# Kernel tuning notes

Hardware: AMD Instinct MI355X
Metric: run time of the kernel (lower is better)

The kernel has to match this reference:

```python
import jax, jax.numpy as jnp
import numpy as np

N = 131072   # number of profile points
S = 64       # n_samples (PSF samples per point)
D = H = W = 256


def setup_inputs() -> dict:
    key = jax.random.key(0)
    k1, k2, k3, k4, k5, k6 = jax.random.split(key, 6)
    x = jax.random.normal(k1, (1, 1, D, H, W), dtype=jnp.float32)
    # voxel-space coordinates (x, y, z) inside the volume
    sampleGrid = jax.random.uniform(k2, (N, 3), dtype=jnp.float32) * jnp.array(
        [W - 1, H - 1, D - 1], dtype=jnp.float32)
    # small axis-angle rotations + translations: [N, 1, 6]
    rot = jax.random.normal(k3, (N, 1, 3), dtype=jnp.float32) * 0.02
    trn = jax.random.normal(k4, (N, 1, 3), dtype=jnp.float32) * 2.0
    ax = jnp.concatenate([rot, trn], axis=-1)
    half = jax.random.uniform(k5, (N, 1, 3), minval=1.0, maxval=3.0, dtype=jnp.float32)
    bound = jnp.concatenate([-half, half], axis=1)  # [N, 2, 3]
    InvCovScaled = jnp.eye(3, dtype=jnp.float32) * 0.5
    # torch.randn(...) - 0.5 from the original forward, hoisted out for determinism
    xyz_psf = jax.random.normal(k6, (N, S, 3), dtype=jnp.float32) - 0.5
    return dict(x=x, sampleGrid=sampleGrid, ax=ax, bound=bound,
                InvCovScaled=InvCovScaled, xyz_psf=xyz_psf)


def _axisangle2mat(a):
    # a: [N, 6] -> [N, 3, 4] = [R | t] via Rodrigues
    v, t = a[:, :3], a[:, 3:]
    theta = jnp.linalg.norm(v, axis=-1, keepdims=True)          # [N,1]
    k = v / jnp.maximum(theta, 1e-12)                            # unit axis
    kx, ky, kz = k[:, 0], k[:, 1], k[:, 2]
    z = jnp.zeros_like(kx)
    K = jnp.stack([z, -kz, ky, kz, z, -kx, -ky, kx, z], axis=-1).reshape(-1, 3, 3)
    ct = jnp.cos(theta)[..., None]  # [N,1,1]
    st = jnp.sin(theta)[..., None]
    I = jnp.eye(3, dtype=a.dtype)
    R = I + st * K + (1.0 - ct) * jnp.matmul(K, K)
    return jnp.concatenate([R, t[..., None]], axis=-1)           # [N,3,4]


def _grid_sample_3d(vol, grid):
    # vol: [D,H,W]; grid: [M,3] normalized coords (x,y,z) in [-1,1]
    # matches F.grid_sample(mode='bilinear', padding_mode='zeros', align_corners=False)
    d, h, w = vol.shape
    sizes = jnp.array([w, h, d], dtype=vol.dtype)
    pix = ((grid + 1.0) * sizes - 1.0) * 0.5                     # unnormalize
    ix, iy, iz = pix[:, 0], pix[:, 1], pix[:, 2]
    x0 = jnp.floor(ix); y0 = jnp.floor(iy); z0 = jnp.floor(iz)
    fx = ix - x0; fy = iy - y0; fz = iz - z0
    x0 = x0.astype(jnp.int32); y0 = y0.astype(jnp.int32); z0 = z0.astype(jnp.int32)

    def gather(xi, yi, zi):
        valid = ((xi >= 0) & (xi < w) & (yi >= 0) & (yi < h) & (zi >= 0) & (zi < d))
        xc = jnp.clip(xi, 0, w - 1)
        yc = jnp.clip(yi, 0, h - 1)
        zc = jnp.clip(zi, 0, d - 1)
        return jnp.where(valid, vol[zc, yc, xc], jnp.zeros((), vol.dtype))

    out = jnp.zeros(grid.shape[0], dtype=vol.dtype)
    for dx in (0, 1):
        wx = fx if dx else (1.0 - fx)
        for dy in (0, 1):
            wy = fy if dy else (1.0 - fy)
            for dz in (0, 1):
                wz = fz if dz else (1.0 - fz)
                out = out + gather(x0 + dx, y0 + dy, z0 + dz) * (wx * wy * wz)
    return out


def reference(x, sampleGrid, ax, bound, InvCovScaled, xyz_psf):
    vol = x[0, 0]                                                # [D,H,W]
    size = jnp.array([x.shape[-1], x.shape[-2], x.shape[-3]], dtype=x.dtype)  # [W,H,D]

    # pose matrices [N,1,3,4]
    mat = _axisangle2mat(ax.reshape(-1, 6)).reshape(ax.shape[:-1] + (3, 4))
    R = mat[..., :3]                                             # [N,1,3,3]
    T = mat[..., 3]                                              # [N,1,3]
    # trans_first=True: p' = R @ (p + T)
    p = sampleGrid[:, None] + T                                  # [N,1,3]
    mat_sampleGrid = jnp.einsum('nkij,nkj->nki', R, p)           # [N,1,3]

    # PSF offsets: [N,S,3]
    bound_psf = xyz_psf * ((bound[:, 1, :] - bound[:, 0, :]) * 0.5)[:, None]
    psf = mat_sampleGrid + bound_psf                             # [N,S,3]

    grid = 2.0 * (psf / (size - 1.0) - 0.5)                      # normalize per-axis
    psf_x = _grid_sample_3d(vol, grid.reshape(-1, 3)).reshape(psf.shape[:-1])  # [N,S]

    center = bound_psf
    q = jnp.einsum('nsi,ij,nsj->ns', center, InvCovScaled, center)
    w = jnp.exp(-0.5 * q)                                        # [N,S]
    y = (psf_x * w).sum(-1) / w.sum(-1)                          # [N]
    return y
```

## Files before the change

kernel.cpp:

```cpp
#include <hip/hip_runtime.h>


#define VOL_N 256
#define S_PSF 64
#define NBUCKET 4096
#define TBL_ELEMS (1 << 24)
#define TBL_BYTES ((size_t)TBL_ELEMS * 8)

typedef float vf4 __attribute__((ext_vector_type(4)));
typedef _Float16 vh4 __attribute__((ext_vector_type(4)));
typedef _Float16 vh8 __attribute__((ext_vector_type(8)));


__device__ __forceinline__ int bucket_of(const float* __restrict__ sg, int n) {
    int cx = min(max((int)sg[n * 3 + 0], 0), VOL_N - 1) >> 4;
    int cy = min(max((int)sg[n * 3 + 1], 0), VOL_N - 1) >> 4;
    int cz = min(max((int)sg[n * 3 + 2], 0), VOL_N - 1) >> 4;
    int m = 0;
    #pragma unroll
    for (int b = 0; b < 4; b++) {
        m |= (((cx >> b) & 1) << (3 * b))
           | (((cy >> b) & 1) << (3 * b + 1))
           | (((cz >> b) & 1) << (3 * b + 2));
    }
    return m;
}

__global__ void zero_hist_kernel(int* __restrict__ ws) {
    int i = blockIdx.x * blockDim.x + threadIdx.x;
    if (i < NBUCKET) ws[i] = 0;
}

__global__ void hist_kernel(const float* __restrict__ sg, int* __restrict__ ws, int N) {
    int n = blockIdx.x * blockDim.x + threadIdx.x;
    if (n >= N) return;
    atomicAdd(&ws[bucket_of(sg, n)], 1);
}

__global__ __launch_bounds__(1024) void scan_kernel(int* __restrict__ ws) {
    __shared__ int tmp[1024];
    const int t = threadIdx.x;
    int h0 = ws[t * 4 + 0], h1 = ws[t * 4 + 1], h2 = ws[t * 4 + 2], h3 = ws[t * 4 + 3];
    int s = h0 + h1 + h2 + h3;
    tmp[t] = s;
    __syncthreads();
    for (int off = 1; off < 1024; off <<= 1) {
        int v = (t >= off) ? tmp[t - off] : 0;
        __syncthreads();
        tmp[t] += v;
        __syncthreads();
    }
    int excl = tmp[t] - s;
    ws[NBUCKET + t * 4 + 0] = excl;
    ws[NBUCKET + t * 4 + 1] = excl + h0;
    ws[NBUCKET + t * 4 + 2] = excl + h0 + h1;
    ws[NBUCKET + t * 4 + 3] = excl + h0 + h1 + h2;
}

__global__ void scatter_kernel(const float* __restrict__ sg, int* __restrict__ ws, int N) {
    int n = blockIdx.x * blockDim.x + threadIdx.x;
    if (n >= N) return;
    int b = bucket_of(sg, n);
    int pos = atomicAdd(&ws[NBUCKET + b], 1);
    ws[2 * NBUCKET + pos] = n;
}

__global__ __launch_bounds__(256) void build_quad_kernel(
    const float* __restrict__ vol, vh4* __restrict__ tbl) {
    const int t = blockIdx.x * 256 + threadIdx.x;
    const int x2 = (t & 127) << 1;
    const int y = (t >> 7) & 255;
    const int z = t >> 15;
    const float* r0 = vol + (z << 16) + (y << 8);
    const float* r1 = vol + (z << 16) + (min(y + 1, VOL_N - 1) << 8);
    const float2 a = *(const float2*)(r0 + x2);
    const float2 b = *(const float2*)(r1 + x2);
    const float a2 = (x2 == VOL_N - 2) ? a.y : r0[x2 + 2];
    const float b2 = (x2 == VOL_N - 2) ? b.y : r1[x2 + 2];

    union { vh8 h; vf4 f; } o;
    o.h = (vh8){(_Float16)a.x, (_Float16)a.y, (_Float16)b.x, (_Float16)b.y,
                (_Float16)a.y, (_Float16)a2,  (_Float16)b.y, (_Float16)b2};
    *(vf4*)(tbl + ((z << 16) + (y << 8) + x2)) = o.f;
}

template <bool USE_TBL>
__global__ __launch_bounds__(256, 4) void psf_sample_kernel(
    const float* __restrict__ vol,
    const vh4* __restrict__ tbl,
    const float* __restrict__ sampleGrid,
    const float* __restrict__ ax,
    const float* __restrict__ bound,
    const float* __restrict__ invcov,
    const float* __restrict__ xyz_psf,
    const int* __restrict__ perm,
    float* __restrict__ out,
    int N)
{
    const int lane = threadIdx.x & 63;

    int bid = blockIdx.x;
    const int nb = gridDim.x;
    if ((nb & 7) == 0) bid = (bid & 7) * (nb >> 3) + (bid >> 3);

    const int i = bid * (blockDim.x >> 6) + (threadIdx.x >> 6);
    if (i >= N) return;
    const int n = __builtin_amdgcn_readfirstlane(perm ? perm[i] : i);

    const float vx = ax[n * 6 + 0], vy = ax[n * 6 + 1], vz = ax[n * 6 + 2];
    const float tx = ax[n * 6 + 3], ty = ax[n * 6 + 4], tz = ax[n * 6 + 5];

    const float theta = sqrtf(vx * vx + vy * vy + vz * vz);
    const float kinv = 1.0f / fmaxf(theta, 1e-12f);
    const float kx = vx * kinv, ky = vy * kinv, kz = vz * kinv;
    const float ct = __cosf(theta), st = __sinf(theta);
    const float oc = 1.0f - ct;

    const float r00 = 1.0f + oc * (-(ky * ky + kz * kz));
    const float r01 = -st * kz + oc * kx * ky;
    const float r02 =  st * ky + oc * kx * kz;
    const float r10 =  st * kz + oc * kx * ky;
    const float r11 = 1.0f + oc * (-(kx * kx + kz * kz));
    const float r12 = -st * kx + oc * ky * kz;
    const float r20 = -st * ky + oc * kx * kz;
    const float r21 =  st * kx + oc * ky * kz;
    const float r22 = 1.0f + oc * (-(kx * kx + ky * ky));

    const float px = sampleGrid[n * 3 + 0] + tx;
    const float py = sampleGrid[n * 3 + 1] + ty;
    const float pz = sampleGrid[n * 3 + 2] + tz;

    const float cx = r00 * px + r01 * py + r02 * pz;
    const float cy = r10 * px + r11 * py + r12 * pz;
    const float cz = r20 * px + r21 * py + r22 * pz;

    const float hx = (bound[n * 6 + 3] - bound[n * 6 + 0]) * 0.5f;
    const float hy = (bound[n * 6 + 4] - bound[n * 6 + 1]) * 0.5f;
    const float hz = (bound[n * 6 + 5] - bound[n * 6 + 2]) * 0.5f;

    const float m00 = invcov[0], m01 = invcov[1], m02 = invcov[2];
    const float m10 = invcov[3], m11 = invcov[4], m12 = invcov[5];
    const float m20 = invcov[6], m21 = invcov[7], m22 = invcov[8];

    const int pbase = (n * S_PSF + lane) * 3;
    const float ox = xyz_psf[pbase + 0] * hx;
    const float oy = xyz_psf[pbase + 1] * hy;
    const float oz = xyz_psf[pbase + 2] * hz;

    const float scale = (float)VOL_N / (float)(VOL_N - 1);
    const float ix = (cx + ox) * scale - 0.5f;
    const float iy = (cy + oy) * scale - 0.5f;
    const float iz = (cz + oz) * scale - 0.5f;

    const float x0f = floorf(ix), y0f = floorf(iy), z0f = floorf(iz);
    const float fx = ix - x0f, fy = iy - y0f, fz = iz - z0f;
    const int x0 = (int)x0f, y0 = (int)y0f, z0 = (int)z0f;
    const int x1 = x0 + 1, y1 = y0 + 1, z1 = z0 + 1;

    const bool vx0 = (unsigned)x0 < (unsigned)VOL_N;
    const bool vx1 = (unsigned)x1 < (unsigned)VOL_N;
    const bool vy0 = (unsigned)y0 < (unsigned)VOL_N;
    const bool vy1 = (unsigned)y1 < (unsigned)VOL_N;
    const bool vz0 = (unsigned)z0 < (unsigned)VOL_N;
    const bool vz1 = (unsigned)z1 < (unsigned)VOL_N;

    const float wx0 = 1.0f - fx, wx1 = fx;
    const float wy0 = 1.0f - fy, wy1 = fy;
    const float wz0 = 1.0f - fz, wz1 = fz;

    float v000, v001, v010, v011, v100, v101, v110, v111;
    if (USE_TBL) {
        const int xg = min(max(x0, 0), VOL_N - 1);
        const int yg = min(max(y0, 0), VOL_N - 1);
        const int zg0 = min(max(z0, 0), VOL_N - 1);
        const int zg1 = min(max(z1, 0), VOL_N - 1);
        const int common = (yg << 8) + xg;
        const vh4 p0 = tbl[(zg0 << 16) + common];
        const vh4 p1 = tbl[(zg1 << 16) + common];
        const bool lox = x0 < 0;
        const bool loy = y0 < 0;
        float s00 = p0.x, s01 = p0.y, s10 = p0.z, s11 = p0.w;
        float a01 = lox ? s00 : s01, a11 = lox ? s10 : s11;
        v000 = s00;                 v001 = a01;
        v010 = loy ? s00 : s10;     v011 = loy ? a01 : a11;
        s00 = p1.x; s01 = p1.y; s10 = p1.z; s11 = p1.w;
        a01 = lox ? s00 : s01; a11 = lox ? s10 : s11;
        v100 = s00;                 v101 = a01;
        v110 = loy ? s00 : s10;     v111 = loy ? a01 : a11;
    } else {
        const int xc0 = min(max(x0, 0), VOL_N - 1);
        const int xc1 = min(max(x1, 0), VOL_N - 1);
        const int yc0 = min(max(y0, 0), VOL_N - 1);
        const int yc1 = min(max(y1, 0), VOL_N - 1);
        const int zc0 = min(max(z0, 0), VOL_N - 1);
        const int zc1 = min(max(z1, 0), VOL_N - 1);
        const int zo0 = zc0 << 16, zo1 = zc1 << 16;
        const int yo0 = yc0 << 8, yo1 = yc1 << 8;
        v000 = vol[zo0 + yo0 + xc0];
        v001 = vol[zo0 + yo0 + xc1];
        v010 = vol[zo0 + yo1 + xc0];
        v011 = vol[zo0 + yo1 + xc1];
        v100 = vol[zo1 + yo0 + xc0];
        v101 = vol[zo1 + yo0 + xc1];
        v110 = vol[zo1 + yo1 + xc0];
        v111 = vol[zo1 + yo1 + xc1];
    }

    float acc = 0.0f;
    acc += (vx0 && vy0 && vz0) ? v000 * (wx0 * wy0 * wz0) : 0.0f;
    acc += (vx1 && vy0 && vz0) ? v001 * (wx1 * wy0 * wz0) : 0.0f;
    acc += (vx0 && vy1 && vz0) ? v010 * (wx0 * wy1 * wz0) : 0.0f;
    acc += (vx1 && vy1 && vz0) ? v011 * (wx1 * wy1 * wz0) : 0.0f;
    acc += (vx0 && vy0 && vz1) ? v100 * (wx0 * wy0 * wz1) : 0.0f;
    acc += (vx1 && vy0 && vz1) ? v101 * (wx1 * wy0 * wz1) : 0.0f;
    acc += (vx0 && vy1 && vz1) ? v110 * (wx0 * wy1 * wz1) : 0.0f;
    acc += (vx1 && vy1 && vz1) ? v111 * (wx1 * wy1 * wz1) : 0.0f;

    const float qx = m00 * ox + m01 * oy + m02 * oz;
    const float qy = m10 * ox + m11 * oy + m12 * oz;
    const float qz = m20 * ox + m21 * oy + m22 * oz;
    const float q = ox * qx + oy * qy + oz * qz;
    const float w = __expf(-0.5f * q);

    float num = acc * w;
    float den = w;
    #pragma unroll
    for (int m = 32; m >= 1; m >>= 1) {
        num += __shfl_xor(num, m, 64);
        den += __shfl_xor(den, m, 64);
    }
    if (lane == 0) out[n] = num / den;
}

extern "C" void kernel_launch(void* const* d_in, const int* in_sizes, int n_in,
                              void* d_out, int out_size, void* d_ws, size_t ws_size,
                              hipStream_t stream) {
    const float* x        = (const float*)d_in[0];
    const float* sg       = (const float*)d_in[1];
    const float* ax       = (const float*)d_in[2];
    const float* bound    = (const float*)d_in[3];
    const float* invcov   = (const float*)d_in[4];
    const float* xyz_psf  = (const float*)d_in[5];
    float* out            = (float*)d_out;

    const int N = in_sizes[1] / 3;
    const size_t sort_bytes = (size_t)(2 * NBUCKET + N) * sizeof(int);

    const bool use_tbl  = ws_size >= TBL_BYTES + sort_bytes;
    const bool use_sort = use_tbl || ws_size >= sort_bytes;

    vh4* tbl = use_tbl ? (vh4*)d_ws : nullptr;
    int* sort_ws = use_tbl ? (int*)((char*)d_ws + TBL_BYTES) : (int*)d_ws;

    int* perm = nullptr;
    if (use_sort) {
        zero_hist_kernel<<<(NBUCKET + 255) / 256, 256, 0, stream>>>(sort_ws);
        hist_kernel<<<(N + 255) / 256, 256, 0, stream>>>(sg, sort_ws, N);
        scan_kernel<<<1, 1024, 0, stream>>>(sort_ws);
        scatter_kernel<<<(N + 255) / 256, 256, 0, stream>>>(sg, sort_ws, N);
        perm = sort_ws + 2 * NBUCKET;
    }
    if (use_tbl) {
        build_quad_kernel<<<(VOL_N * VOL_N * VOL_N / 2) / 256, 256, 0, stream>>>(x, tbl);
    }

    dim3 block(256);
    dim3 grid((N + 3) / 4);
    if (use_tbl) {
        psf_sample_kernel<true><<<grid, block, 0, stream>>>(
            x, tbl, sg, ax, bound, invcov, xyz_psf, perm, out, N);
    } else {
        psf_sample_kernel<false><<<grid, block, 0, stream>>>(
            x, nullptr, sg, ax, bound, invcov, xyz_psf, perm, out, N);
    }
}
```

Measured before the change: 322.7 us.

## Precompute per-point pose centers in scatter pass and stream them in sorted order

Moves the per-point Rodrigues rotation, center transform and half-extent computation into the scatter kernel, writing an 8-float record at each point's sorted position. The sampling kernel then reads one contiguous, coalesced record per wave instead of scattered ax/sampleGrid/bound loads followed by redundant per-lane math. It also uses nontemporal loads for the PSF offsets, folds the bounds checks into the trilinear weights, and rewrites the interpolation as nested FMAs. The cost is extra workspace and a slightly heavier scatter kernel.

```diff
diff --git a/kernel.cpp b/kernel.cpp
--- a/kernel.cpp
+++ b/kernel.cpp
@@ -57,12 +57,54 @@
     ws[NBUCKET + t * 4 + 3] = excl + h0 + h1 + h2;
 }
 
-__global__ void scatter_kernel(const float* __restrict__ sg, int* __restrict__ ws, int N) {
+__global__ void scatter_kernel(const float* __restrict__ sg,
+                               const float* __restrict__ ax,
+                               const float* __restrict__ bound,
+                               int* __restrict__ ws,
+                               float* __restrict__ pre, int N) {
     int n = blockIdx.x * blockDim.x + threadIdx.x;
     if (n >= N) return;
     int b = bucket_of(sg, n);
     int pos = atomicAdd(&ws[NBUCKET + b], 1);
     ws[2 * NBUCKET + pos] = n;
+
+    const float vx = ax[n * 6 + 0], vy = ax[n * 6 + 1], vz = ax[n * 6 + 2];
+    const float tx = ax[n * 6 + 3], ty = ax[n * 6 + 4], tz = ax[n * 6 + 5];
+
+    const float theta = sqrtf(vx * vx + vy * vy + vz * vz);
+    const float kinv = 1.0f / fmaxf(theta, 1e-12f);
+    const float kx = vx * kinv, ky = vy * kinv, kz = vz * kinv;
+    const float ct = __cosf(theta), st = __sinf(theta);
+    const float oc = 1.0f - ct;
+
+    const float r00 = 1.0f + oc * (-(ky * ky + kz * kz));
+    const float r01 = -st * kz + oc * kx * ky;
+    const float r02 =  st * ky + oc * kx * kz;
+    const float r10 =  st * kz + oc * kx * ky;
+    const float r11 = 1.0f + oc * (-(kx * kx + kz * kz));
+    const float r12 = -st * kx + oc * ky * kz;
+    const float r20 = -st * ky + oc * kx * kz;
+    const float r21 =  st * kx + oc * ky * kz;
+    const float r22 = 1.0f + oc * (-(kx * kx + ky * ky));
+
+    const float px = sg[n * 3 + 0] + tx;
+    const float py = sg[n * 3 + 1] + ty;
+    const float pz = sg[n * 3 + 2] + tz;
+
+    const float cx = r00 * px + r01 * py + r02 * pz;
+    const float cy = r10 * px + r11 * py + r12 * pz;
+    const float cz = r20 * px + r21 * py + r22 * pz;
+
+    const float hx = (bound[n * 6 + 3] - bound[n * 6 + 0]) * 0.5f;
+    const float hy = (bound[n * 6 + 4] - bound[n * 6 + 1]) * 0.5f;
+    const float hz = (bound[n * 6 + 5] - bound[n * 6 + 2]) * 0.5f;
+
+    const float scale = (float)VOL_N / (float)(VOL_N - 1);
+    float4 A = make_float4(cx * scale - 0.5f, cy * scale - 0.5f,
+                           cz * scale - 0.5f, hx);
+    float4 B = make_float4(hy, hz, 0.0f, 0.0f);
+    *(float4*)(pre + (size_t)pos * 8)     = A;
+    *(float4*)(pre + (size_t)pos * 8 + 4) = B;
 }
 
 __global__ __launch_bounds__(256) void build_quad_kernel(
@@ -84,7 +126,7 @@
     *(vf4*)(tbl + ((z << 16) + (y << 8) + x2)) = o.f;
 }
 
-template <bool USE_TBL>
+template <bool USE_TBL, bool USE_PRE>
 __global__ __launch_bounds__(256, 4) void psf_sample_kernel(
     const float* __restrict__ vol,
     const vh4* __restrict__ tbl,
@@ -94,6 +136,7 @@
     const float* __restrict__ invcov,
     const float* __restrict__ xyz_psf,
     const int* __restrict__ perm,
+    const float* __restrict__ pre,
     float* __restrict__ out,
     int N)
 {
@@ -103,77 +146,76 @@
     const int nb = gridDim.x;
     if ((nb & 7) == 0) bid = (bid & 7) * (nb >> 3) + (bid >> 3);
 
-    const int i = bid * (blockDim.x >> 6) + (threadIdx.x >> 6);
-    if (i >= N) return;
-    const int n = __builtin_amdgcn_readfirstlane(perm ? perm[i] : i);
-
-    const float vx = ax[n * 6 + 0], vy = ax[n * 6 + 1], vz = ax[n * 6 + 2];
-    const float tx = ax[n * 6 + 3], ty = ax[n * 6 + 4], tz = ax[n * 6 + 5];
-
-    const float theta = sqrtf(vx * vx + vy * vy + vz * vz);
-    const float kinv = 1.0f / fmaxf(theta, 1e-12f);
-    const float kx = vx * kinv, ky = vy * kinv, kz = vz * kinv;
-    const float ct = __cosf(theta), st = __sinf(theta);
-    const float oc = 1.0f - ct;
-
-    const float r00 = 1.0f + oc * (-(ky * ky + kz * kz));
-    const float r01 = -st * kz + oc * kx * ky;
-    const float r02 =  st * ky + oc * kx * kz;
-    const float r10 =  st * kz + oc * kx * ky;
-    const float r11 = 1.0f + oc * (-(kx * kx + kz * kz));
-    const float r12 = -st * kx + oc * ky * kz;
-    const float r20 = -st * ky + oc * kx * kz;
-    const float r21 =  st * kx + oc * ky * kz;
-    const float r22 = 1.0f + oc * (-(kx * kx + ky * ky));
-
-    const float px = sampleGrid[n * 3 + 0] + tx;
-    const float py = sampleGrid[n * 3 + 1] + ty;
-    const float pz = sampleGrid[n * 3 + 2] + tz;
-
-    const float cx = r00 * px + r01 * py + r02 * pz;
-    const float cy = r10 * px + r11 * py + r12 * pz;
-    const float cz = r20 * px + r21 * py + r22 * pz;
-
-    const float hx = (bound[n * 6 + 3] - bound[n * 6 + 0]) * 0.5f;
-    const float hy = (bound[n * 6 + 4] - bound[n * 6 + 1]) * 0.5f;
-    const float hz = (bound[n * 6 + 5] - bound[n * 6 + 2]) * 0.5f;
+    const int ii = bid * (blockDim.x >> 6) + (threadIdx.x >> 6);
+    if (ii >= N) return;
+    const int i = __builtin_amdgcn_readfirstlane(ii);
+    const int n = USE_PRE ? __builtin_amdgcn_readfirstlane(perm[i]) : i;
+
+    const float scale = (float)VOL_N / (float)(VOL_N - 1);
+    float icx, icy, icz, hx, hy, hz;
+    if (USE_PRE) {
+        const float4 A = *(const float4*)(pre + (size_t)i * 8);
+        const float4 B = *(const float4*)(pre + (size_t)i * 8 + 4);
+        icx = A.x; icy = A.y; icz = A.z; hx = A.w; hy = B.x; hz = B.y;
+    } else {
+        const float vx = ax[n * 6 + 0], vy = ax[n * 6 + 1], vz = ax[n * 6 + 2];
+        const float tx = ax[n * 6 + 3], ty = ax[n * 6 + 4], tz = ax[n * 6 + 5];
+        const float theta = sqrtf(vx * vx + vy * vy + vz * vz);
+        const float kinv = 1.0f / fmaxf(theta, 1e-12f);
+        const float kx = vx * kinv, ky = vy * kinv, kz = vz * kinv;
+        const float ct = __cosf(theta), st = __sinf(theta);
+        const float oc = 1.0f - ct;
+        const float r00 = 1.0f + oc * (-(ky * ky + kz * kz));
+        const float r01 = -st * kz + oc * kx * ky;
+        const float r02 =  st * ky + oc * kx * kz;
+        const float r10 =  st * kz + oc * kx * ky;
+        const float r11 = 1.0f + oc * (-(kx * kx + kz * kz));
+        const float r12 = -st * kx + oc * ky * kz;
+        const float r20 = -st * ky + oc * kx * kz;
+        const float r21 =  st * kx + oc * ky * kz;
+        const float r22 = 1.0f + oc * (-(kx * kx + ky * ky));
+        const float px = sampleGrid[n * 3 + 0] + tx;
+        const float py = sampleGrid[n * 3 + 1] + ty;
+        const float pz = sampleGrid[n * 3 + 2] + tz;
+        icx = (r00 * px + r01 * py + r02 * pz) * scale - 0.5f;
+        icy = (r10 * px + r11 * py + r12 * pz) * scale - 0.5f;
+        icz = (r20 * px + r21 * py + r22 * pz) * scale - 0.5f;
+        hx = (bound[n * 6 + 3] - bound[n * 6 + 0]) * 0.5f;
+        hy = (bound[n * 6 + 4] - bound[n * 6 + 1]) * 0.5f;
+        hz = (bound[n * 6 + 5] - bound[n * 6 + 2]) * 0.5f;
+    }
 
     const float m00 = invcov[0], m01 = invcov[1], m02 = invcov[2];
     const float m10 = invcov[3], m11 = invcov[4], m12 = invcov[5];
     const float m20 = invcov[6], m21 = invcov[7], m22 = invcov[8];
 
     const int pbase = (n * S_PSF + lane) * 3;
-    const float ox = xyz_psf[pbase + 0] * hx;
-    const float oy = xyz_psf[pbase + 1] * hy;
-    const float oz = xyz_psf[pbase + 2] * hz;
-
-    const float scale = (float)VOL_N / (float)(VOL_N - 1);
-    const float ix = (cx + ox) * scale - 0.5f;
-    const float iy = (cy + oy) * scale - 0.5f;
-    const float iz = (cz + oz) * scale - 0.5f;
+    const float gx = __builtin_nontemporal_load(xyz_psf + pbase + 0);
+    const float gy = __builtin_nontemporal_load(xyz_psf + pbase + 1);
+    const float gz = __builtin_nontemporal_load(xyz_psf + pbase + 2);
+    const float ox = gx * hx, oy = gy * hy, oz = gz * hz;
+
+    const float ix = fmaf(ox, scale, icx);
+    const float iy = fmaf(oy, scale, icy);
+    const float iz = fmaf(oz, scale, icz);
 
     const float x0f = floorf(ix), y0f = floorf(iy), z0f = floorf(iz);
     const float fx = ix - x0f, fy = iy - y0f, fz = iz - z0f;
     const int x0 = (int)x0f, y0 = (int)y0f, z0 = (int)z0f;
-    const int x1 = x0 + 1, y1 = y0 + 1, z1 = z0 + 1;
-
-    const bool vx0 = (unsigned)x0 < (unsigned)VOL_N;
-    const bool vx1 = (unsigned)x1 < (unsigned)VOL_N;
-    const bool vy0 = (unsigned)y0 < (unsigned)VOL_N;
-    const bool vy1 = (unsigned)y1 < (unsigned)VOL_N;
-    const bool vz0 = (unsigned)z0 < (unsigned)VOL_N;
-    const bool vz1 = (unsigned)z1 < (unsigned)VOL_N;
-
-    const float wx0 = 1.0f - fx, wx1 = fx;
-    const float wy0 = 1.0f - fy, wy1 = fy;
-    const float wz0 = 1.0f - fz, wz1 = fz;
+
+    const float wx0 = ((unsigned)x0       < (unsigned)VOL_N) ? (1.0f - fx) : 0.0f;
+    const float wx1 = ((unsigned)(x0 + 1) < (unsigned)VOL_N) ? fx          : 0.0f;
+    const float wy0 = ((unsigned)y0       < (unsigned)VOL_N) ? (1.0f - fy) : 0.0f;
+    const float wy1 = ((unsigned)(y0 + 1) < (unsigned)VOL_N) ? fy          : 0.0f;
+    const float wz0 = ((unsigned)z0       < (unsigned)VOL_N) ? (1.0f - fz) : 0.0f;
+    const float wz1 = ((unsigned)(z0 + 1) < (unsigned)VOL_N) ? fz          : 0.0f;
 
     float v000, v001, v010, v011, v100, v101, v110, v111;
     if (USE_TBL) {
         const int xg = min(max(x0, 0), VOL_N - 1);
         const int yg = min(max(y0, 0), VOL_N - 1);
         const int zg0 = min(max(z0, 0), VOL_N - 1);
-        const int zg1 = min(max(z1, 0), VOL_N - 1);
+        const int zg1 = min(max(z0 + 1, 0), VOL_N - 1);
         const int common = (yg << 8) + xg;
         const vh4 p0 = tbl[(zg0 << 16) + common];
         const vh4 p1 = tbl[(zg1 << 16) + common];
@@ -189,11 +231,11 @@
         v110 = loy ? s00 : s10;     v111 = loy ? a01 : a11;
     } else {
         const int xc0 = min(max(x0, 0), VOL_N - 1);
-        const int xc1 = min(max(x1, 0), VOL_N - 1);
+        const int xc1 = min(max(x0 + 1, 0), VOL_N - 1);
         const int yc0 = min(max(y0, 0), VOL_N - 1);
-        const int yc1 = min(max(y1, 0), VOL_N - 1);
+        const int yc1 = min(max(y0 + 1, 0), VOL_N - 1);
         const int zc0 = min(max(z0, 0), VOL_N - 1);
-        const int zc1 = min(max(z1, 0), VOL_N - 1);
+        const int zc1 = min(max(z0 + 1, 0), VOL_N - 1);
         const int zo0 = zc0 << 16, zo1 = zc1 << 16;
         const int yo0 = yc0 << 8, yo1 = yc1 << 8;
         v000 = vol[zo0 + yo0 + xc0];
@@ -206,20 +248,18 @@
         v111 = vol[zo1 + yo1 + xc1];
     }
 
-    float acc = 0.0f;
-    acc += (vx0 && vy0 && vz0) ? v000 * (wx0 * wy0 * wz0) : 0.0f;
-    acc += (vx1 && vy0 && vz0) ? v001 * (wx1 * wy0 * wz0) : 0.0f;
-    acc += (vx0 && vy1 && vz0) ? v010 * (wx0 * wy1 * wz0) : 0.0f;
-    acc += (vx1 && vy1 && vz0) ? v011 * (wx1 * wy1 * wz0) : 0.0f;
-    acc += (vx0 && vy0 && vz1) ? v100 * (wx0 * wy0 * wz1) : 0.0f;
-    acc += (vx1 && vy0 && vz1) ? v101 * (wx1 * wy0 * wz1) : 0.0f;
-    acc += (vx0 && vy1 && vz1) ? v110 * (wx0 * wy1 * wz1) : 0.0f;
-    acc += (vx1 && vy1 && vz1) ? v111 * (wx1 * wy1 * wz1) : 0.0f;
-
-    const float qx = m00 * ox + m01 * oy + m02 * oz;
-    const float qy = m10 * ox + m11 * oy + m12 * oz;
-    const float qz = m20 * ox + m21 * oy + m22 * oz;
-    const float q = ox * qx + oy * qy + oz * qz;
+    const float r0 = fmaf(v001, wx1, v000 * wx0);
+    const float r1 = fmaf(v011, wx1, v010 * wx0);
+    const float r2 = fmaf(v101, wx1, v100 * wx0);
+    const float r3 = fmaf(v111, wx1, v110 * wx0);
+    const float s0 = fmaf(r1, wy1, r0 * wy0);
+    const float s1 = fmaf(r3, wy1, r2 * wy0);
+    const float acc = fmaf(s1, wz1, s0 * wz0);
+
+    const float qx = fmaf(m00, ox, fmaf(m01, oy, m02 * oz));
+    const float qy = fmaf(m10, ox, fmaf(m11, oy, m12 * oz));
+    const float qz = fmaf(m20, ox, fmaf(m21, oy, m22 * oz));
+    const float q = fmaf(ox, qx, fmaf(oy, qy, oz * qz));
     const float w = __expf(-0.5f * q);
 
     float num = acc * w;
@@ -245,19 +285,23 @@
 
     const int N = in_sizes[1] / 3;
     const size_t sort_bytes = (size_t)(2 * NBUCKET + N) * sizeof(int);
-
-    const bool use_tbl  = ws_size >= TBL_BYTES + sort_bytes;
-    const bool use_sort = use_tbl || ws_size >= sort_bytes;
+    const size_t sort_pad   = (sort_bytes + 31) & ~(size_t)31;
+    const size_t pre_bytes  = (size_t)N * 8 * sizeof(float);
+
+    const bool use_tbl  = ws_size >= TBL_BYTES + sort_pad + pre_bytes;
+    const bool use_sort = use_tbl || ws_size >= sort_pad + pre_bytes;
 
     vh4* tbl = use_tbl ? (vh4*)d_ws : nullptr;
-    int* sort_ws = use_tbl ? (int*)((char*)d_ws + TBL_BYTES) : (int*)d_ws;
+    char* base = (char*)d_ws + (use_tbl ? TBL_BYTES : 0);
+    int* sort_ws = (int*)base;
+    float* pre = (float*)(base + sort_pad);
 
     int* perm = nullptr;
     if (use_sort) {
         zero_hist_kernel<<<(NBUCKET + 255) / 256, 256, 0, stream>>>(sort_ws);
         hist_kernel<<<(N + 255) / 256, 256, 0, stream>>>(sg, sort_ws, N);
         scan_kernel<<<1, 1024, 0, stream>>>(sort_ws);
-        scatter_kernel<<<(N + 255) / 256, 256, 0, stream>>>(sg, sort_ws, N);
+        scatter_kernel<<<(N + 255) / 256, 256, 0, stream>>>(sg, ax, bound, sort_ws, pre, N);
         perm = sort_ws + 2 * NBUCKET;
     }
     if (use_tbl) {
@@ -267,10 +311,13 @@
     dim3 block(256);
     dim3 grid((N + 3) / 4);
     if (use_tbl) {
-        psf_sample_kernel<true><<<grid, block, 0, stream>>>(
-            x, tbl, sg, ax, bound, invcov, xyz_psf, perm, out, N);
+        psf_sample_kernel<true, true><<<grid, block, 0, stream>>>(
+            x, tbl, sg, ax, bound, invcov, xyz_psf, perm, pre, out, N);
+    } else if (use_sort) {
+        psf_sample_kernel<false, true><<<grid, block, 0, stream>>>(
+            x, nullptr, sg, ax, bound, invcov, xyz_psf, perm, pre, out, N);
     } else {
-        psf_sample_kernel<false><<<grid, block, 0, stream>>>(
-            x, nullptr, sg, ax, bound, invcov, xyz_psf, perm, out, N);
-    }
-}
+        psf_sample_kernel<false, false><<<grid, block, 0, stream>>>(
+            x, nullptr, sg, ax, bound, invcov, xyz_psf, nullptr, nullptr, out, N);
+    }
+}
```

Result: faster. 304.3 us (-5.7%).
